# Optimization experiments

Hardware: AMD Instinct MI355X
Metric: run time of the kernel (lower is better)

## Reference

```python
import jax, jax.numpy as jnp
import numpy as np

N_NODES = 16384
HIDDEN = 128
N_SPECIES = 119


def setup_inputs() -> dict:
    key = jax.random.key(0)
    k1, k2, k3, k4 = jax.random.split(key, 4)
    h_prev = jax.random.normal(k1, (N_NODES, HIDDEN), dtype=jnp.float32)
    m_curr = jax.random.normal(k2, (N_NODES, HIDDEN), dtype=jnp.float32)
    # sorted species indices (fast indexed_linear path in the original module)
    atom_types = jnp.sort(jax.random.randint(k3, (N_NODES,), 0, N_SPECIES))
    # per-species weight, init randn / sqrt(hidden_dim) as in the torch module
    weight = jax.random.normal(k4, (N_SPECIES, HIDDEN * HIDDEN), dtype=jnp.float32) / jnp.sqrt(
        jnp.float32(HIDDEN)
    )
    return {"h_prev": h_prev, "m_curr": m_curr, "atom_types": atom_types, "weight": weight}


def reference(h_prev, m_curr, atom_types, weight):
    # h_new[i] = h_prev[i] + W[Z[i]] @ m_curr[i]
    D = h_prev.shape[-1]
    W = weight.reshape(weight.shape[0], D, D)        # (S, D, D)
    Wg = W[atom_types]                               # (N, D, D) indexed gather
    m_transformed = jnp.einsum("nij,nj->ni", Wg, m_curr)
    return h_prev + m_transformed
```

## Files before the change

kernel.cpp:

```cpp
#include <hip/hip_runtime.h>
#include <hip/hip_bf16.h>
#include <stdint.h>

#define HID 128
#define TILE_M 64
#define LDS_PAD 8
#define ROW_STRIDE (HID + LDS_PAD)

typedef __attribute__((ext_vector_type(8))) __bf16 bf16x8;
typedef __attribute__((ext_vector_type(4))) float floatx4;

__device__ inline unsigned short f32_to_bf16_rn(float f) {
    union { float f; unsigned int u; } v; v.f = f;
    unsigned int u = v.u;
    unsigned int r = u + 0x7FFFu + ((u >> 16) & 1u);
    return (unsigned short)(r >> 16);
}

__global__ __launch_bounds__(256) void elem_update_kernel(
    const float* __restrict__ h_prev,
    const float* __restrict__ m_curr,
    const int* __restrict__ atom_types,
    const float* __restrict__ weight,
    float* __restrict__ out)
{
    __shared__ unsigned short m_lds[TILE_M * ROW_STRIDE];
    __shared__ unsigned short w_lds[HID * ROW_STRIDE];
    __shared__ int types_lds[TILE_M];

    const int tid  = threadIdx.x;
    const int n0   = blockIdx.x * TILE_M;
    const int lane = tid & 63;
    const int wave = tid >> 6;
    const int l15  = lane & 15;
    const int quad = lane >> 4;

    if (tid < TILE_M) types_lds[tid] = atom_types[n0 + tid];

    {
        const float4* src = (const float4*)(m_curr + (size_t)n0 * HID);
        #pragma unroll
        for (int it = 0; it < (TILE_M * (HID / 4)) / 256; ++it) {
            int c    = tid + it * 256;
            int row  = c >> 5;
            int col4 = c & 31;
            float4 v = src[row * (HID / 4) + col4];
            unsigned short b[4] = { f32_to_bf16_rn(v.x), f32_to_bf16_rn(v.y),
                                    f32_to_bf16_rn(v.z), f32_to_bf16_rn(v.w) };
            *(uint2*)(&m_lds[row * ROW_STRIDE + col4 * 4]) = *(const uint2*)b;
        }
    }
    __syncthreads();

    int s = 0;
    while (s < TILE_M) {
        const int z = types_lds[s];
        int e = s + 1;
        while (e < TILE_M && types_lds[e] == z) ++e;

        {
            const float4* wsrc = (const float4*)(weight + (size_t)z * HID * HID);
            #pragma unroll
            for (int it = 0; it < (HID * (HID / 4)) / 256; ++it) {
                int c    = tid + it * 256;
                int row  = c >> 5;
                int col4 = c & 31;
                float4 v = wsrc[row * (HID / 4) + col4];
                unsigned short b[4] = { f32_to_bf16_rn(v.x), f32_to_bf16_rn(v.y),
                                        f32_to_bf16_rn(v.z), f32_to_bf16_rn(v.w) };
                *(uint2*)(&w_lds[row * ROW_STRIDE + col4 * 4]) = *(const uint2*)b;
            }
        }
        __syncthreads();

        const int r0 = wave * 16;
        if (r0 < e && r0 + 16 > s) {
            floatx4 acc[8];
            #pragma unroll
            for (int nt = 0; nt < 8; ++nt) acc[nt] = (floatx4)(0.0f);

            #pragma unroll
            for (int kk = 0; kk < 4; ++kk) {
                bf16x8 a = *(const bf16x8*)(&m_lds[(r0 + l15) * ROW_STRIDE + kk * 32 + quad * 8]);
                #pragma unroll
                for (int nt = 0; nt < 8; ++nt) {
                    bf16x8 b = *(const bf16x8*)(&w_lds[(nt * 16 + l15) * ROW_STRIDE + kk * 32 + quad * 8]);
                    acc[nt] = __builtin_amdgcn_mfma_f32_16x16x32_bf16(a, b, acc[nt], 0, 0, 0);
                }
            }

            #pragma unroll
            for (int nt = 0; nt < 8; ++nt) {
                #pragma unroll
                for (int r = 0; r < 4; ++r) {
                    int row = r0 + quad * 4 + r;
                    if (row >= s && row < e) {
                        int node = n0 + row;
                        int col  = nt * 16 + l15;
                        size_t idx = (size_t)node * HID + col;
                        out[idx] = h_prev[idx] + acc[nt][r];
                    }
                }
            }
        }
        s = e;
        __syncthreads();
    }
}

extern "C" void kernel_launch(void* const* d_in, const int* in_sizes, int n_in,
                              void* d_out, int out_size, void* d_ws, size_t ws_size,
                              hipStream_t stream) {
    const float* h_prev     = (const float*)d_in[0];
    const float* m_curr     = (const float*)d_in[1];
    const int*   atom_types = (const int*)d_in[2];
    const float* weight     = (const float*)d_in[3];
    float*       out        = (float*)d_out;

    const int n_nodes = in_sizes[2];
    const int blocks  = n_nodes / TILE_M;

    elem_update_kernel<<<blocks, 256, 0, stream>>>(h_prev, m_curr, atom_types, weight, out);
}
```

Measured before the change: 95.26 us.

## Drop LDS staging; each wave computes a 16x32 tile straight from global memory

Removes shared-memory staging of the m and W tiles along with all block barriers. Each wave now owns a 16-row by 32-column output tile and loads its fp32 operands directly from global memory, converting them to bf16 in registers. Runs of equal species are found with a shuffle and a ballot, and h_prev is preloaded into the accumulator so no separate add is needed. This trades LDS reuse for far more redundant global and L2 reads: m rows are reloaded by four waves, and W is reread for every 16-row tile and every species segment.

```diff
diff --git a/kernel.cpp b/kernel.cpp
--- a/kernel.cpp
+++ b/kernel.cpp
@@ -3,9 +3,6 @@
 #include <stdint.h>
 
 #define HID 128
-#define TILE_M 64
-#define LDS_PAD 8
-#define ROW_STRIDE (HID + LDS_PAD)
 
 typedef __attribute__((ext_vector_type(8))) __bf16 bf16x8;
 typedef __attribute__((ext_vector_type(4))) float floatx4;
@@ -17,94 +14,77 @@
     return (unsigned short)(r >> 16);
 }
 
-__global__ __launch_bounds__(256) void elem_update_kernel(
+__device__ inline bf16x8 load_cvt8(const float* __restrict__ p) {
+    float4 v0 = *(const float4*)(p);
+    float4 v1 = *(const float4*)(p + 4);
+    unsigned short b[8] = {
+        f32_to_bf16_rn(v0.x), f32_to_bf16_rn(v0.y), f32_to_bf16_rn(v0.z), f32_to_bf16_rn(v0.w),
+        f32_to_bf16_rn(v1.x), f32_to_bf16_rn(v1.y), f32_to_bf16_rn(v1.z), f32_to_bf16_rn(v1.w)
+    };
+    return *(const bf16x8*)b;
+}
+
+__global__ __launch_bounds__(256, 4) void elem_update_kernel(
     const float* __restrict__ h_prev,
     const float* __restrict__ m_curr,
     const int* __restrict__ atom_types,
     const float* __restrict__ weight,
     float* __restrict__ out)
 {
-    __shared__ unsigned short m_lds[TILE_M * ROW_STRIDE];
-    __shared__ unsigned short w_lds[HID * ROW_STRIDE];
-    __shared__ int types_lds[TILE_M];
-
     const int tid  = threadIdx.x;
-    const int n0   = blockIdx.x * TILE_M;
     const int lane = tid & 63;
     const int wave = tid >> 6;
     const int l15  = lane & 15;
     const int quad = lane >> 4;
 
-    if (tid < TILE_M) types_lds[tid] = atom_types[n0 + tid];
+    const int wg       = blockIdx.x * 4 + wave;
+    const int row_tile = wg >> 2;
+    const int cq       = wg & 3;
+    const int r0       = row_tile * 16;
+    const int c0       = cq * 32;
 
-    {
-        const float4* src = (const float4*)(m_curr + (size_t)n0 * HID);
-        #pragma unroll
-        for (int it = 0; it < (TILE_M * (HID / 4)) / 256; ++it) {
-            int c    = tid + it * 256;
-            int row  = c >> 5;
-            int col4 = c & 31;
-            float4 v = src[row * (HID / 4) + col4];
-            unsigned short b[4] = { f32_to_bf16_rn(v.x), f32_to_bf16_rn(v.y),
-                                    f32_to_bf16_rn(v.z), f32_to_bf16_rn(v.w) };
-            *(uint2*)(&m_lds[row * ROW_STRIDE + col4 * 4]) = *(const uint2*)b;
-        }
-    }
-    __syncthreads();
+    const int t = atom_types[r0 + l15];
 
     int s = 0;
-    while (s < TILE_M) {
-        const int z = types_lds[s];
-        int e = s + 1;
-        while (e < TILE_M && types_lds[e] == z) ++e;
+    while (s < 16) {
+        const int z = __shfl(t, s);
+        unsigned long long neq = __ballot(t != z);
+        unsigned bits = (unsigned)(neq & 0xFFFFull) & ~((1u << (s + 1)) - 1u);
+        const int e = bits ? (int)__builtin_ctz(bits) : 16;
 
-        {
-            const float4* wsrc = (const float4*)(weight + (size_t)z * HID * HID);
+        const float* __restrict__ Wz = weight + (size_t)z * HID * HID;
+
+        floatx4 acc[2];
+        #pragma unroll
+        for (int nt = 0; nt < 2; ++nt) {
             #pragma unroll
-            for (int it = 0; it < (HID * (HID / 4)) / 256; ++it) {
-                int c    = tid + it * 256;
-                int row  = c >> 5;
-                int col4 = c & 31;
-                float4 v = wsrc[row * (HID / 4) + col4];
-                unsigned short b[4] = { f32_to_bf16_rn(v.x), f32_to_bf16_rn(v.y),
-                                        f32_to_bf16_rn(v.z), f32_to_bf16_rn(v.w) };
-                *(uint2*)(&w_lds[row * ROW_STRIDE + col4 * 4]) = *(const uint2*)b;
+            for (int r = 0; r < 4; ++r) {
+                acc[nt][r] = h_prev[(size_t)(r0 + quad * 4 + r) * HID + c0 + nt * 16 + l15];
             }
         }
-        __syncthreads();
 
-        const int r0 = wave * 16;
-        if (r0 < e && r0 + 16 > s) {
-            floatx4 acc[8];
+        #pragma unroll
+        for (int kk = 0; kk < 4; ++kk) {
+            bf16x8 a = load_cvt8(m_curr + (size_t)(r0 + l15) * HID + kk * 32 + quad * 8);
             #pragma unroll
-            for (int nt = 0; nt < 8; ++nt) acc[nt] = (floatx4)(0.0f);
+            for (int nt = 0; nt < 2; ++nt) {
+                bf16x8 b = load_cvt8(Wz + (size_t)(c0 + nt * 16 + l15) * HID + kk * 32 + quad * 8);
+                acc[nt] = __builtin_amdgcn_mfma_f32_16x16x32_bf16(a, b, acc[nt], 0, 0, 0);
+            }
+        }
 
+        #pragma unroll
+        for (int nt = 0; nt < 2; ++nt) {
             #pragma unroll
-            for (int kk = 0; kk < 4; ++kk) {
-                bf16x8 a = *(const bf16x8*)(&m_lds[(r0 + l15) * ROW_STRIDE + kk * 32 + quad * 8]);
-                #pragma unroll
-                for (int nt = 0; nt < 8; ++nt) {
-                    bf16x8 b = *(const bf16x8*)(&w_lds[(nt * 16 + l15) * ROW_STRIDE + kk * 32 + quad * 8]);
-                    acc[nt] = __builtin_amdgcn_mfma_f32_16x16x32_bf16(a, b, acc[nt], 0, 0, 0);
-                }
-            }
-
-            #pragma unroll
-            for (int nt = 0; nt < 8; ++nt) {
-                #pragma unroll
-                for (int r = 0; r < 4; ++r) {
-                    int row = r0 + quad * 4 + r;
-                    if (row >= s && row < e) {
-                        int node = n0 + row;
-                        int col  = nt * 16 + l15;
-                        size_t idx = (size_t)node * HID + col;
-                        out[idx] = h_prev[idx] + acc[nt][r];
-                    }
+            for (int r = 0; r < 4; ++r) {
+                int row = quad * 4 + r;
+                if (row >= s && row < e) {
+                    size_t idx = (size_t)(r0 + row) * HID + c0 + nt * 16 + l15;
+                    out[idx] = acc[nt][r];
                 }
             }
         }
         s = e;
-        __syncthreads();
     }
 }
 
@@ -118,7 +98,6 @@
     float*       out        = (float*)d_out;
 
     const int n_nodes = in_sizes[2];
-    const int blocks  = n_nodes / TILE_M;
-
+    const int blocks  = n_nodes / 16;
     elem_update_kernel<<<blocks, 256, 0, stream>>>(h_prev, m_curr, atom_types, weight, out);
 }
```

Measured after the change: 87.07 us. 1.09x faster.
